# Optimization experiments

Measured on AMD Instinct MI355X. Metric: run time of the kernel, lower is better.

The kernel has to match this reference:

```python
import jax, jax.numpy as jnp
import numpy as np
import math

G = 128          # graphs per batch
N_PER = 512      # nodes per graph (equal-size, contiguous layout)
N = G * N_PER    # 65536 nodes
DEG = 16
E = N * DEG      # 1,048,576 edges
IN_C, HID, OUT_C = 100, 128, 2
RATIO = 0.8
EPS = 1e-5

K1 = int(math.ceil(RATIO * N_PER))  # 410
K2 = int(math.ceil(RATIO * K1))     # 328
K3 = int(math.ceil(RATIO * K2))     # 263


def gcn_conv(x, src, dst, emask, W, b):
    # GCNConv: linear, symmetric deg^-1/2 norm with self-loops, scatter-add
    xl = x @ W
    n = x.shape[0]
    w = emask.astype(x.dtype)
    deg = jnp.ones((n,), x.dtype).at[dst].add(w)      # +1 from self loop
    dinv = jax.lax.rsqrt(deg)
    coef = dinv[src] * dinv[dst] * w                  # [E]
    out = jnp.zeros_like(xl).at[dst].add(coef[:, None] * xl[src])
    out = out + (dinv * dinv)[:, None] * xl           # self-loop messages
    return out + b


def batch_norm(x, gamma, beta):
    # BatchNorm1d over node dim (training-mode batch statistics)
    mu = x.mean(0)
    var = x.var(0)
    return (x - mu) * jax.lax.rsqrt(var + EPS) * gamma + beta


def topk_pool(x, src, dst, emask, att, g, n, k):
    # TopKPooling: score = tanh(x@att/||att||), keep top-k per graph, gate features,
    # drop edges touching removed nodes (via validity mask).
    score = jnp.tanh((x @ att) / jnp.linalg.norm(att))
    _, idx = jax.lax.top_k(score.reshape(g, n), k)           # [g,k] local ids
    kept = (idx + (jnp.arange(g) * n)[:, None]).reshape(-1)   # global ids
    new_x = x[kept] * score[kept][:, None]
    old2new = jnp.full((g * n,), -1, jnp.int32).at[kept].set(
        jnp.arange(g * k, dtype=jnp.int32))
    s2, d2 = old2new[src], old2new[dst]
    valid = emask & (s2 >= 0) & (d2 >= 0)
    return new_x, jnp.maximum(s2, 0), jnp.maximum(d2, 0), valid


def readout(x, g, k):
    # [global_max_pool, global_mean_pool] over each graph's k nodes
    xr = x.reshape(g, k, -1)
    return jnp.concatenate([xr.max(1), xr.mean(1)], axis=1)   # [g, 2C]


def setup_inputs() -> dict:
    key = jax.random.key(0)
    ks = jax.random.split(key, 16)
    x = jax.random.normal(ks[0], (N, IN_C), jnp.float32)
    # within-graph random edges, then offset by graph id
    e_per = E // G
    local = jax.random.randint(ks[1], (2, G, e_per), 0, N_PER)
    edge_index = (local + (jnp.arange(G) * N_PER)[None, :, None]).reshape(2, E).astype(jnp.int32)
    batch = jnp.repeat(jnp.arange(G, dtype=jnp.int32), N_PER)

    def w(k, fi, fo):
        return jax.random.normal(k, (fi, fo), jnp.float32) * (1.0 / np.sqrt(fi))

    z = lambda c: jnp.zeros((c,), jnp.float32)
    o = lambda c: jnp.ones((c,), jnp.float32)
    return {
        'x': x, 'edge_index': edge_index, 'batch': batch,
        'Wp': w(ks[2], IN_C, 128), 'bp': z(128),
        'W1': w(ks[3], 128, HID), 'b1': z(HID), 'g1': o(HID), 'be1': z(HID),
        'att1': jax.random.normal(ks[4], (HID,), jnp.float32),
        'W2': w(ks[5], HID, HID), 'b2': z(HID), 'g2': o(HID), 'be2': z(HID),
        'att2': jax.random.normal(ks[6], (HID,), jnp.float32),
        'W3': w(ks[7], HID, HID), 'b3': z(HID), 'g3': o(HID), 'be3': z(HID),
        'att3': jax.random.normal(ks[8], (HID,), jnp.float32),
        'Wl1': w(ks[9], 2 * HID, HID), 'bl1': z(HID),
        'Wl2': w(ks[10], HID, OUT_C), 'bl2': z(OUT_C),
    }


def reference(x, edge_index, batch, Wp, bp, W1, b1, g1, be1, att1,
              W2, b2, g2, be2, att2, W3, b3, g3, be3, att3,
              Wl1, bl1, Wl2, bl2):
    src, dst = edge_index[0], edge_index[1]
    emask = jnp.ones((E,), bool)
    h = jax.nn.relu(x @ Wp + bp)

    h = jax.nn.relu(batch_norm(gcn_conv(h, src, dst, emask, W1, b1), g1, be1))
    h, src, dst, emask = topk_pool(h, src, dst, emask, att1, G, N_PER, K1)
    x1 = readout(h, G, K1)

    h = jax.nn.relu(batch_norm(gcn_conv(h, src, dst, emask, W2, b2), g2, be2))
    h, src, dst, emask = topk_pool(h, src, dst, emask, att2, G, K1, K2)
    x2 = readout(h, G, K2)

    h = jax.nn.relu(batch_norm(gcn_conv(h, src, dst, emask, W3, b3), g3, be3))
    h, src, dst, emask = topk_pool(h, src, dst, emask, att3, G, K2, K3)
    x3 = readout(h, G, K3)

    s = x1 + x2 + x3                       # [G, 2*HID]
    s = jax.nn.relu(s @ Wl1 + bl1)
    return s @ Wl2 + bl2                   # [G, OUT_C]
```

## Files before the change

### kernel.cpp

```cpp
#include <hip/hip_runtime.h>
#include <math.h>

#define G     128
#define NPER  512
#define NTOT  65536
#define E_TOT 1048576
#define EPG   8192
#define INC   100
#define HID   128
#define KP1   410
#define KP2   328
#define KP3   263

__global__ void init_kernel(short* __restrict__ cmap, float* __restrict__ sread,
                            float* __restrict__ bnpart) {
    int t = blockIdx.x * 256 + threadIdx.x;
    if (t < NTOT) cmap[t] = (short)(t & (NPER - 1));
    if (t < G * 256) { sread[t] = 0.f; bnpart[t] = 0.f; }
}

__global__ __launch_bounds__(512, 2) void csr_build0(
    const int* __restrict__ src, const int* __restrict__ dst,
    unsigned short* __restrict__ csr_g, int* __restrict__ rowptr_g)
{
    __shared__ int cnt_s[NPER];
    __shared__ int rowptr_s[NPER + 1];
    __shared__ int wo_s[NPER];
    __shared__ int chunksum_s[9];

    const int g = blockIdx.x, tid = threadIdx.x, lane = tid & 63, wv = tid >> 6;
    const int ebase = g * EPG, obase = g * NPER;

    cnt_s[tid] = 0;
    __syncthreads();
    for (int e = tid; e < EPG; e += 512)
        atomicAdd(&cnt_s[dst[ebase + e] - obase], 1);
    __syncthreads();

    int v = cnt_s[tid], x = v;
#pragma unroll
    for (int d = 1; d < 64; d <<= 1) {
        int y = __shfl_up(x, d);
        if (lane >= d) x += y;
    }
    if (lane == 63) chunksum_s[wv] = x;
    __syncthreads();
    if (tid == 0) {
        int acc = 0;
#pragma unroll
        for (int k = 0; k < 8; ++k) { int t = chunksum_s[k]; chunksum_s[k] = acc; acc += t; }
    }
    __syncthreads();
    int excl = x - v + chunksum_s[wv];
    rowptr_s[tid] = excl; wo_s[tid] = excl;
    if (tid == 511) rowptr_s[512] = excl + v;
    __syncthreads();

    for (int i = tid; i <= NPER; i += 512) rowptr_g[g * 513 + i] = rowptr_s[i];
    for (int e = tid; e < EPG; e += 512) {
        int sl = src[ebase + e] - obase, dl = dst[ebase + e] - obase;
        int pos = atomicAdd(&wo_s[dl], 1);
        csr_g[g * EPG + pos] = (unsigned short)sl;
    }
}

template<int K, bool RELU>
__global__ __launch_bounds__(256, 2) void gemm_kernel(
    const float* __restrict__ A, const float* __restrict__ W,
    const float* __restrict__ bias, float* __restrict__ out, int M)
{
    constexpr int KC = 32;
    __shared__ float Ws[KC][128];
    __shared__ float As[KC][132];
    const int tid  = threadIdx.x;
    const int row0 = blockIdx.x * 128;
    const int r0 = (tid >> 4) * 8;
    const int c0 = (tid & 15) * 8;

    float acc[8][8];
#pragma unroll
    for (int i = 0; i < 8; ++i)
#pragma unroll
        for (int j = 0; j < 8; ++j) acc[i][j] = 0.f;

    for (int k0 = 0; k0 < K; k0 += KC) {
        const int kc  = (K - k0 < KC) ? (K - k0) : KC;
        const int nf4 = kc >> 2;

        for (int i = tid; i < kc * 32; i += 256) {
            int kk = i >> 5, c4 = i & 31;
            *((float4*)&Ws[kk][0] + c4) =
                *((const float4*)(W + (size_t)(k0 + kk) * 128) + c4);
        }
        for (int i = tid; i < nf4 * 128; i += 256) {
            int row = i / nf4, f4 = i - row * nf4;
            float4 v = *(const float4*)(A + (size_t)(row0 + row) * K + k0 + f4 * 4);
            As[f4 * 4 + 0][row] = v.x;
            As[f4 * 4 + 1][row] = v.y;
            As[f4 * 4 + 2][row] = v.z;
            As[f4 * 4 + 3][row] = v.w;
        }
        __syncthreads();

        for (int kk = 0; kk < kc; ++kk) {
            float4 b0 = *(const float4*)&Ws[kk][c0];
            float4 b1 = *(const float4*)&Ws[kk][c0 + 4];
            float4 a0 = *(const float4*)&As[kk][r0];
            float4 a1 = *(const float4*)&As[kk][r0 + 4];
            float a[8] = {a0.x, a0.y, a0.z, a0.w, a1.x, a1.y, a1.z, a1.w};
            float b[8] = {b0.x, b0.y, b0.z, b0.w, b1.x, b1.y, b1.z, b1.w};
#pragma unroll
            for (int i = 0; i < 8; ++i)
#pragma unroll
                for (int j = 0; j < 8; ++j)
                    acc[i][j] += a[i] * b[j];
        }
        __syncthreads();
    }

#pragma unroll
    for (int i = 0; i < 8; ++i) {
        int row = row0 + r0 + i;
        float o[8];
#pragma unroll
        for (int j = 0; j < 8; ++j) {
            float v = acc[i][j];
            if (RELU) v = fmaxf(v + bias[c0 + j], 0.f);
            o[j] = v;
        }
        float* po = out + (size_t)row * 128 + c0;
        *(float4*)po       = make_float4(o[0], o[1], o[2], o[3]);
        *(float4*)(po + 4) = make_float4(o[4], o[5], o[6], o[7]);
    }
}

template<int NCUR>
__global__ __launch_bounds__(256, 8) void gather_kernel(
    const float* __restrict__ xs, const unsigned short* __restrict__ csr_g,
    const int* __restrict__ rowptr_g, const float* __restrict__ bvec,
    float* __restrict__ out, float* __restrict__ bnpart)
{
    constexpr int CHUNK = (NCUR + 15) / 16;
    constexpr int CSRCAP = 1536;
    __shared__ int   rowptr_s[NCUR + 1];
    __shared__ float dinv_s[NCUR];
    __shared__ unsigned short csr_s[CSRCAP];
    __shared__ float red_s[512];

    const int g = blockIdx.x, s = blockIdx.y;
    const int tid = threadIdx.x, lane = tid & 63, w = tid >> 6;
    const int nbase = g * NCUR;
    const int d0 = s * CHUNK;
    const int d1 = (d0 + CHUNK < NCUR) ? d0 + CHUNK : NCUR;

    const int* rp = rowptr_g + g * 513;
    for (int i = tid; i <= NCUR; i += 256) rowptr_s[i] = rp[i];
    __syncthreads();
    for (int i = tid; i < NCUR; i += 256)
        dinv_s[i] = rsqrtf((float)(rowptr_s[i + 1] - rowptr_s[i] + 1));

    const int base = rowptr_s[d0];
    int nume = rowptr_s[d1] - base;
    if (nume > CSRCAP) nume = CSRCAP;
    const unsigned short* cg = csr_g + g * EPG + base;
    for (int i = tid; i < nume; i += 256) csr_s[i] = cg[i];
    __syncthreads();

    const float2* x2 = (const float2*)xs;
    float2* o2p = (float2*)out;
    const float2 b2 = ((const float2*)bvec)[lane];
    float2 sum = make_float2(0.f, 0.f), sq = make_float2(0.f, 0.f);

    for (int da = d0 + w; da < d1; da += 8) {
        const int db = da + 4;
        const bool hb = db < d1;
        const int ia = rowptr_s[da] - base;
        const int na = rowptr_s[da + 1] - rowptr_s[da];
        const int ib = hb ? rowptr_s[db] - base : 0;
        const int nbl = hb ? rowptr_s[db + 1] - rowptr_s[db] : 0;
        const float dva = dinv_s[da];
        const float dvb = hb ? dinv_s[db] : 0.f;

        float2 xa = x2[(size_t)(nbase + da) * 64 + lane];
        float2 accA = make_float2(dva * xa.x, dva * xa.y);
        float2 accB = make_float2(0.f, 0.f);
        if (hb) {
            float2 xb = x2[(size_t)(nbase + db) * 64 + lane];
            accB = make_float2(dvb * xb.x, dvb * xb.y);
        }

        const int nmin = na < nbl ? na : nbl;
#pragma unroll 2
        for (int t = 0; t < nmin; ++t) {
            int sa = csr_s[ia + t], sb = csr_s[ib + t];
            float wa = dinv_s[sa], wb = dinv_s[sb];
            float2 va = x2[(size_t)(nbase + sa) * 64 + lane];
            float2 vb = x2[(size_t)(nbase + sb) * 64 + lane];
            accA.x += wa * va.x; accA.y += wa * va.y;
            accB.x += wb * vb.x; accB.y += wb * vb.y;
        }
#pragma unroll 4
        for (int t = nmin; t < na; ++t) {
            int sa = csr_s[ia + t];
            float wa = dinv_s[sa];
            float2 va = x2[(size_t)(nbase + sa) * 64 + lane];
            accA.x += wa * va.x; accA.y += wa * va.y;
        }
#pragma unroll 4
        for (int t = nmin; t < nbl; ++t) {
            int sb = csr_s[ib + t];
            float wb = dinv_s[sb];
            float2 vb = x2[(size_t)(nbase + sb) * 64 + lane];
            accB.x += wb * vb.x; accB.y += wb * vb.y;
        }

        float2 oA = make_float2(b2.x + dva * accA.x, b2.y + dva * accA.y);
        o2p[(size_t)(nbase + da) * 64 + lane] = oA;
        sum.x += oA.x; sum.y += oA.y;
        sq.x  += oA.x * oA.x; sq.y += oA.y * oA.y;
        if (hb) {
            float2 oB = make_float2(b2.x + dvb * accB.x, b2.y + dvb * accB.y);
            o2p[(size_t)(nbase + db) * 64 + lane] = oB;
            sum.x += oB.x; sum.y += oB.y;
            sq.x  += oB.x * oB.x; sq.y += oB.y * oB.y;
        }
    }

    float2* red2 = (float2*)red_s;
    red2[tid] = sum; __syncthreads();
    if (tid < 64) {
        float2 a = red2[tid], b_ = red2[tid + 64],
               c = red2[tid + 128], d_ = red2[tid + 192];
        atomicAdd(&bnpart[g * 256 + 2 * tid],     a.x + b_.x + c.x + d_.x);
        atomicAdd(&bnpart[g * 256 + 2 * tid + 1], a.y + b_.y + c.y + d_.y);
    }
    __syncthreads();
    red2[tid] = sq; __syncthreads();
    if (tid < 64) {
        float2 a = red2[tid], b_ = red2[tid + 64],
               c = red2[tid + 128], d_ = red2[tid + 192];
        atomicAdd(&bnpart[g * 256 + 128 + 2 * tid],     a.x + b_.x + c.x + d_.x);
        atomicAdd(&bnpart[g * 256 + 128 + 2 * tid + 1], a.y + b_.y + c.y + d_.y);
    }
}

__global__ __launch_bounds__(1024, 1) void bnfin_kernel(
    const float* __restrict__ bnpart, float n,
    const float* __restrict__ gamma, const float* __restrict__ beta,
    const float* __restrict__ att, float* __restrict__ coefs)
{
    __shared__ float ssum[8][128];
    __shared__ float ssq[8][128];
    __shared__ float r[128];
    const int t = threadIdx.x & 127, slice = threadIdx.x >> 7;
    float s = 0.f, q = 0.f;
    for (int g = slice; g < G; g += 8) {
        s += bnpart[g * 256 + t];
        q += bnpart[g * 256 + 128 + t];
    }
    ssum[slice][t] = s; ssq[slice][t] = q;
    if (threadIdx.x < 128) { float av = att[t]; r[t] = av * av; }
    __syncthreads();
    if (threadIdx.x < 128) {
        float S = 0.f, Q = 0.f;
#pragma unroll
        for (int k = 0; k < 8; ++k) { S += ssum[k][t]; Q += ssq[k][t]; }
        for (int st = 64; st > 0; st >>= 1) {
            if (t < st) r[t] += r[t + st];
            __syncthreads();
        }
        float norm = sqrtf(r[0]);
        float mu   = S / n;
        float var  = Q / n - mu * mu;
        float inv  = rsqrtf(var + 1e-5f);
        float a    = gamma[t] * inv;
        coefs[t]        = a;
        coefs[128 + t]  = beta[t] - mu * a;
        coefs[256 + t]  = att[t] / norm;
    }
}

template<int NCUR, int KK, bool BUILD>
__global__ __launch_bounds__(1024, 1) void pool_kernel(
    const float* __restrict__ gcn, const float* __restrict__ coefs,
    float* __restrict__ newx, short* __restrict__ cmap,
    float* __restrict__ sread, float* __restrict__ bnpart,
    const int* __restrict__ src, const int* __restrict__ dst,
    unsigned short* __restrict__ csr_g, int* __restrict__ rowptr_g)
{
    __shared__ float score_s[NCUR];
    __shared__ unsigned long long key_s[NCUR];
    __shared__ short o2n_s[NCUR];
    __shared__ unsigned short n2o_s[KK];
    __shared__ short cmap_s[NPER];
    __shared__ float2 red2[1024];
    __shared__ int   cnt_s[512];
    __shared__ int   rowptr_s[513];
    __shared__ int   wo_s[512];
    __shared__ int   chunksum_s[9];

    const int g = blockIdx.x, tid = threadIdx.x, lane = tid & 63, w = tid >> 6;
    const int nb = g * NCUR;
    const int ebase = g * EPG, obase = g * NPER;
    const float a0 = coefs[lane],       a1 = coefs[64 + lane];
    const float c0 = coefs[128 + lane], c1 = coefs[192 + lane];
    const float t0 = coefs[256 + lane], t1 = coefs[320 + lane];

    for (int i = tid; i < NPER; i += 1024) cmap_s[i] = cmap[obase + i];

    for (int i = w; i < NCUR; i += 16) {
        const float* row = gcn + (size_t)(nb + i) * 128;
        float h0 = fmaxf(a0 * row[lane] + c0, 0.f);
        float h1 = fmaxf(a1 * row[64 + lane] + c1, 0.f);
        float p  = h0 * t0 + h1 * t1;
#pragma unroll
        for (int off = 32; off > 0; off >>= 1) p += __shfl_down(p, off);
        if (lane == 0) score_s[i] = tanhf(p);
    }
    __syncthreads();

    for (int i = tid; i < NCUR; i += 1024) {
        unsigned u   = __float_as_uint(score_s[i]);
        unsigned key = (u & 0x80000000u) ? ~u : (u | 0x80000000u);
        key_s[i] = ((unsigned long long)key << 32) |
                   (unsigned long long)(0xFFFFFFFFu - (unsigned)i);
    }
    __syncthreads();

    for (int i = tid; i < NCUR; i += 1024) {
        const unsigned long long ki = key_s[i];
        int r = 0;
#pragma unroll 8
        for (int j = 0; j < NCUR; ++j) r += (key_s[j] > ki) ? 1 : 0;
        o2n_s[i] = (r < KK) ? (short)r : (short)-1;
        if (r < KK) n2o_s[r] = (unsigned short)i;
    }
    __syncthreads();

    float mx0 = -1e30f, mx1 = -1e30f, sm0 = 0.f, sm1 = 0.f;
    for (int j2 = w; j2 < KK; j2 += 16) {
        int old = n2o_s[j2];
        float s = score_s[old];
        const float* row = gcn + (size_t)(nb + old) * 128;
        float h0 = fmaxf(a0 * row[lane] + c0, 0.f) * s;
        float h1 = fmaxf(a1 * row[64 + lane] + c1, 0.f) * s;
        float* orow = newx + (size_t)(g * KK + j2) * 128;
        orow[lane]      = h0;
        orow[64 + lane] = h1;
        mx0 = fmaxf(mx0, h0); mx1 = fmaxf(mx1, h1);
        sm0 += h0; sm1 += h1;
    }
    red2[tid] = make_float2(mx0, mx1);
    __syncthreads();
    if (tid < 64) {
        float m = -1e30f;
#pragma unroll
        for (int w2 = 0; w2 < 16; ++w2) m = fmaxf(m, red2[w2 * 64 + tid].x);
        sread[g * 256 + tid] += m;
    } else if (tid < 128) {
        int l = tid - 64;
        float m = -1e30f;
#pragma unroll
        for (int w2 = 0; w2 < 16; ++w2) m = fmaxf(m, red2[w2 * 64 + l].y);
        sread[g * 256 + tid] += m;
    }
    __syncthreads();
    red2[tid] = make_float2(sm0, sm1);
    __syncthreads();
    if (tid < 64) {
        float sm = 0.f;
#pragma unroll
        for (int w2 = 0; w2 < 16; ++w2) sm += red2[w2 * 64 + tid].x;
        sread[g * 256 + 128 + tid] += sm * (1.0f / KK);
    } else if (tid < 128) {
        int l = tid - 64;
        float sm = 0.f;
#pragma unroll
        for (int w2 = 0; w2 < 16; ++w2) sm += red2[w2 * 64 + l].y;
        sread[g * 256 + 128 + tid] += sm * (1.0f / KK);
    }

    for (int o = tid; o < NPER; o += 1024) {
        int m = cmap_s[o];
        short nm = (m >= 0) ? o2n_s[m] : (short)-1;
        cmap_s[o] = nm;
        cmap[obase + o] = nm;
    }
    if (tid < 256) bnpart[g * 256 + tid] = 0.f;

    if (!BUILD) return;
    __syncthreads();

    if (tid < 512) cnt_s[tid] = 0;
    __syncthreads();
    for (int e = tid; e < EPG; e += 1024) {
        int sl = cmap_s[src[ebase + e] - obase];
        int dl = cmap_s[dst[ebase + e] - obase];
        if ((sl | dl) >= 0) atomicAdd(&cnt_s[dl], 1);
    }
    __syncthreads();
    int v = 0, x = 0;
    if (tid < 512) {
        v = cnt_s[tid]; x = v;
#pragma unroll
        for (int d = 1; d < 64; d <<= 1) {
            int y = __shfl_up(x, d);
            if (lane >= d) x += y;
        }
        if (lane == 63) chunksum_s[w] = x;
    }
    __syncthreads();
    if (tid == 0) {
        int acc = 0;
#pragma unroll
        for (int k = 0; k < 8; ++k) { int t = chunksum_s[k]; chunksum_s[k] = acc; acc += t; }
    }
    __syncthreads();
    if (tid < 512) {
        int excl = x - v + chunksum_s[w];
        rowptr_s[tid] = excl; wo_s[tid] = excl;
        if (tid == 511) rowptr_s[512] = excl + v;
    }
    __syncthreads();
    for (int i = tid; i <= 512; i += 1024) rowptr_g[g * 513 + i] = rowptr_s[i];
    for (int e = tid; e < EPG; e += 1024) {
        int sl = cmap_s[src[ebase + e] - obase];
        int dl = cmap_s[dst[ebase + e] - obase];
        if ((sl | dl) >= 0) {
            int pos = atomicAdd(&wo_s[dl], 1);
            csr_g[g * EPG + pos] = (unsigned short)sl;
        }
    }
}

__global__ void final_kernel(const float* __restrict__ sread,
                             const float* __restrict__ Wl1,
                             const float* __restrict__ bl1,
                             const float* __restrict__ Wl2,
                             const float* __restrict__ bl2,
                             float* __restrict__ out)
{
    __shared__ float s_s[256];
    __shared__ float hid_s[128];
    int g = blockIdx.x, t = threadIdx.x;
    s_s[t]       = sread[g * 256 + t];
    s_s[128 + t] = sread[g * 256 + 128 + t];
    __syncthreads();
    float acc = bl1[t];
    for (int i = 0; i < 256; ++i) acc += s_s[i] * Wl1[i * 128 + t];
    hid_s[t] = fmaxf(acc, 0.f);
    __syncthreads();
    if (t < 2) {
        float o = bl2[t];
        for (int j = 0; j < 128; ++j) o += hid_s[j] * Wl2[j * 2 + t];
        out[g * 2 + t] = o;
    }
}

extern "C" void kernel_launch(void* const* d_in, const int* in_sizes, int n_in,
                              void* d_out, int out_size, void* d_ws, size_t ws_size,
                              hipStream_t stream)
{
    const float* x    = (const float*)d_in[0];
    const int*   ei   = (const int*)d_in[1];
    const float* Wp   = (const float*)d_in[3];
    const float* bp   = (const float*)d_in[4];
    const float* W1   = (const float*)d_in[5];
    const float* b1   = (const float*)d_in[6];
    const float* g1   = (const float*)d_in[7];
    const float* be1  = (const float*)d_in[8];
    const float* att1 = (const float*)d_in[9];
    const float* W2   = (const float*)d_in[10];
    const float* b2   = (const float*)d_in[11];
    const float* g2   = (const float*)d_in[12];
    const float* be2  = (const float*)d_in[13];
    const float* att2 = (const float*)d_in[14];
    const float* W3   = (const float*)d_in[15];
    const float* b3   = (const float*)d_in[16];
    const float* g3   = (const float*)d_in[17];
    const float* be3  = (const float*)d_in[18];
    const float* att3 = (const float*)d_in[19];
    const float* Wl1  = (const float*)d_in[20];
    const float* bl1  = (const float*)d_in[21];
    const float* Wl2  = (const float*)d_in[22];
    const float* bl2  = (const float*)d_in[23];
    float* out = (float*)d_out;

    const int* srcp = ei;
    const int* dstp = ei + E_TOT;

    char* ws = (char*)d_ws;
    float*          bufA   = (float*)ws;
    float*          bufB   = (float*)(ws + 33554432);
    unsigned short* csr    = (unsigned short*)(ws + 67108864);
    int*            rowptr = (int*)  (ws + 69206016);
    float*          bnpart = (float*)(ws + 69468672);
    short*          cmap   = (short*)(ws + 69599744);
    float*          sread  = (float*)(ws + 69730816);
    float*          coefs  = (float*)(ws + 69861888);

    init_kernel<<<256, 256, 0, stream>>>(cmap, sread, bnpart);
    csr_build0<<<G, 512, 0, stream>>>(srcp, dstp, csr, rowptr);

    gemm_kernel<INC, true><<<512, 256, 0, stream>>>(x, Wp, bp, bufA, NTOT);

    gemm_kernel<128, false><<<512, 256, 0, stream>>>(bufA, W1, nullptr, bufB, NTOT);
    gather_kernel<512><<<dim3(G, 16), 256, 0, stream>>>(bufB, csr, rowptr, b1, bufA, bnpart);
    bnfin_kernel<<<1, 1024, 0, stream>>>(bnpart, (float)NTOT, g1, be1, att1, coefs);
    pool_kernel<512, KP1, true><<<G, 1024, 0, stream>>>(bufA, coefs, bufB, cmap, sread, bnpart,
                                                        srcp, dstp, csr, rowptr);

    gemm_kernel<128, false><<<410, 256, 0, stream>>>(bufB, W2, nullptr, bufA, G * KP1);
    gather_kernel<KP1><<<dim3(G, 16), 256, 0, stream>>>(bufA, csr, rowptr, b2, bufB, bnpart);
    bnfin_kernel<<<1, 1024, 0, stream>>>(bnpart, (float)(G * KP1), g2, be2, att2, coefs);
    pool_kernel<KP1, KP2, true><<<G, 1024, 0, stream>>>(bufB, coefs, bufA, cmap, sread, bnpart,
                                                        srcp, dstp, csr, rowptr);

    gemm_kernel<128, false><<<328, 256, 0, stream>>>(bufA, W3, nullptr, bufB, G * KP2);
    gather_kernel<KP2><<<dim3(G, 16), 256, 0, stream>>>(bufB, csr, rowptr, b3, bufA, bnpart);
    bnfin_kernel<<<1, 1024, 0, stream>>>(bnpart, (float)(G * KP2), g3, be3, att3, coefs);
    pool_kernel<KP2, KP3, false><<<G, 1024, 0, stream>>>(bufA, coefs, bufB, cmap, sread, bnpart,
                                                         srcp, dstp, csr, rowptr);

    final_kernel<<<G, 128, 0, stream>>>(sread, Wl1, bl1, Wl2, bl2, out);
}
```

Measured before the change: 493.0 us.

## Fold source-side degree norm into GEMM epilogue, fuse BN finalize into pool, double-buffer GEMM

```diff
diff --git a/kernel.cpp b/kernel.cpp
--- a/kernel.cpp
+++ b/kernel.cpp
@@ -16,7 +16,8 @@
                             float* __restrict__ bnpart) {
     int t = blockIdx.x * 256 + threadIdx.x;
     if (t < NTOT) cmap[t] = (short)(t & (NPER - 1));
-    if (t < G * 256) { sread[t] = 0.f; bnpart[t] = 0.f; }
+    if (t < G * 256) sread[t] = 0.f;
+    if (t < 3 * G * 256) bnpart[t] = 0.f;
 }
 
 __global__ __launch_bounds__(512, 2) void csr_build0(
@@ -64,12 +65,11 @@
     }
 }
 
-template<int K, bool RELU>
-__global__ __launch_bounds__(256, 2) void gemm_kernel(
+__global__ __launch_bounds__(256, 2) void gemm_pre(
     const float* __restrict__ A, const float* __restrict__ W,
     const float* __restrict__ bias, float* __restrict__ out, int M)
 {
-    constexpr int KC = 32;
+    constexpr int K = INC, KC = 32;
     __shared__ float Ws[KC][128];
     __shared__ float As[KC][132];
     const int tid  = threadIdx.x;
@@ -102,6 +102,7 @@
         }
         __syncthreads();
 
+#pragma unroll 4
         for (int kk = 0; kk < kc; ++kk) {
             float4 b0 = *(const float4*)&Ws[kk][c0];
             float4 b1 = *(const float4*)&Ws[kk][c0 + 4];
@@ -123,11 +124,127 @@
         int row = row0 + r0 + i;
         float o[8];
 #pragma unroll
-        for (int j = 0; j < 8; ++j) {
-            float v = acc[i][j];
-            if (RELU) v = fmaxf(v + bias[c0 + j], 0.f);
-            o[j] = v;
-        }
+        for (int j = 0; j < 8; ++j)
+            o[j] = fmaxf(acc[i][j] + bias[c0 + j], 0.f);
+        float* po = out + (size_t)row * 128 + c0;
+        *(float4*)po       = make_float4(o[0], o[1], o[2], o[3]);
+        *(float4*)(po + 4) = make_float4(o[4], o[5], o[6], o[7]);
+    }
+}
+
+template<int NCUR>
+__global__ __launch_bounds__(256, 2) void gemm128(
+    const float* __restrict__ A, const float* __restrict__ W,
+    const int* __restrict__ rowptr_g, float* __restrict__ out)
+{
+    constexpr int KC = 32;
+    __shared__ float Ws[2][KC][128];
+    __shared__ float As[2][KC][132];
+    __shared__ float dinv_ls[128];
+    const int tid  = threadIdx.x;
+    const int row0 = blockIdx.x * 128;
+    const int r0 = (tid >> 4) * 8;
+    const int c0 = (tid & 15) * 8;
+
+    if (tid < 128) {
+        int row = row0 + tid;
+        int gg = row / NCUR, ll = row - gg * NCUR;
+        const int* rp = rowptr_g + gg * 513 + ll;
+        dinv_ls[tid] = rsqrtf((float)(rp[1] - rp[0] + 1));
+    }
+
+    const float4* W4 = (const float4*)W;
+
+#pragma unroll
+    for (int j = 0; j < 4; ++j) {
+        int i = tid + j * 256;
+        int kk = i >> 5, c4 = i & 31;
+        *((float4*)&Ws[0][kk][0] + c4) = W4[kk * 32 + c4];
+    }
+#pragma unroll
+    for (int j = 0; j < 4; ++j) {
+        int i = tid + j * 256;
+        int row = i >> 3, f4 = i & 7;
+        float4 v = *(const float4*)(A + (size_t)(row0 + row) * 128 + f4 * 4);
+        As[0][f4 * 4 + 0][row] = v.x;
+        As[0][f4 * 4 + 1][row] = v.y;
+        As[0][f4 * 4 + 2][row] = v.z;
+        As[0][f4 * 4 + 3][row] = v.w;
+    }
+    __syncthreads();
+
+    float acc[8][8];
+#pragma unroll
+    for (int i = 0; i < 8; ++i)
+#pragma unroll
+        for (int j = 0; j < 8; ++j) acc[i][j] = 0.f;
+
+    int p = 0;
+    for (int k0 = 0; k0 < 128; k0 += KC) {
+        const int kn = k0 + KC;
+        const bool has = kn < 128;
+
+        float4 wreg[4], areg[4];
+        if (has) {
+#pragma unroll
+            for (int j = 0; j < 4; ++j) {
+                int i = tid + j * 256;
+                int kk = i >> 5, c4 = i & 31;
+                wreg[j] = W4[(kn + kk) * 32 + c4];
+            }
+#pragma unroll
+            for (int j = 0; j < 4; ++j) {
+                int i = tid + j * 256;
+                int row = i >> 3, f4 = i & 7;
+                areg[j] = *(const float4*)(A + (size_t)(row0 + row) * 128 + kn + f4 * 4);
+            }
+        }
+
+#pragma unroll 4
+        for (int kk = 0; kk < KC; ++kk) {
+            float4 b0 = *(const float4*)&Ws[p][kk][c0];
+            float4 b1 = *(const float4*)&Ws[p][kk][c0 + 4];
+            float4 a0 = *(const float4*)&As[p][kk][r0];
+            float4 a1 = *(const float4*)&As[p][kk][r0 + 4];
+            float a[8] = {a0.x, a0.y, a0.z, a0.w, a1.x, a1.y, a1.z, a1.w};
+            float b[8] = {b0.x, b0.y, b0.z, b0.w, b1.x, b1.y, b1.z, b1.w};
+#pragma unroll
+            for (int i = 0; i < 8; ++i)
+#pragma unroll
+                for (int j = 0; j < 8; ++j)
+                    acc[i][j] += a[i] * b[j];
+        }
+
+        if (has) {
+            int q = p ^ 1;
+#pragma unroll
+            for (int j = 0; j < 4; ++j) {
+                int i = tid + j * 256;
+                int kk = i >> 5, c4 = i & 31;
+                *((float4*)&Ws[q][kk][0] + c4) = wreg[j];
+            }
+#pragma unroll
+            for (int j = 0; j < 4; ++j) {
+                int i = tid + j * 256;
+                int row = i >> 3, f4 = i & 7;
+                float4 v = areg[j];
+                As[q][f4 * 4 + 0][row] = v.x;
+                As[q][f4 * 4 + 1][row] = v.y;
+                As[q][f4 * 4 + 2][row] = v.z;
+                As[q][f4 * 4 + 3][row] = v.w;
+            }
+        }
+        __syncthreads();
+        p ^= 1;
+    }
+
+#pragma unroll
+    for (int i = 0; i < 8; ++i) {
+        int row = row0 + r0 + i;
+        float dv = dinv_ls[r0 + i];
+        float o[8];
+#pragma unroll
+        for (int j = 0; j < 8; ++j) o[j] = acc[i][j] * dv;
         float* po = out + (size_t)row * 128 + c0;
         *(float4*)po       = make_float4(o[0], o[1], o[2], o[3]);
         *(float4*)(po + 4) = make_float4(o[4], o[5], o[6], o[7]);
@@ -142,8 +259,7 @@
 {
     constexpr int CHUNK = (NCUR + 15) / 16;
     constexpr int CSRCAP = 1536;
-    __shared__ int   rowptr_s[NCUR + 1];
-    __shared__ float dinv_s[NCUR];
+    __shared__ int   rowptr_s[CHUNK + 1];
     __shared__ unsigned short csr_s[CSRCAP];
     __shared__ float red_s[512];
 
@@ -152,21 +268,20 @@
     const int nbase = g * NCUR;
     const int d0 = s * CHUNK;
     const int d1 = (d0 + CHUNK < NCUR) ? d0 + CHUNK : NCUR;
-
-    const int* rp = rowptr_g + g * 513;
-    for (int i = tid; i <= NCUR; i += 256) rowptr_s[i] = rp[i];
-    __syncthreads();
-    for (int i = tid; i < NCUR; i += 256)
-        dinv_s[i] = rsqrtf((float)(rowptr_s[i + 1] - rowptr_s[i] + 1));
-
-    const int base = rowptr_s[d0];
-    int nume = rowptr_s[d1] - base;
+    const int len = d1 - d0;
+
+    const int* rp = rowptr_g + g * 513 + d0;
+    for (int i = tid; i <= len; i += 256) rowptr_s[i] = rp[i];
+    __syncthreads();
+
+    const int base = rowptr_s[0];
+    int nume = rowptr_s[len] - base;
     if (nume > CSRCAP) nume = CSRCAP;
     const unsigned short* cg = csr_g + g * EPG + base;
     for (int i = tid; i < nume; i += 256) csr_s[i] = cg[i];
     __syncthreads();
 
-    const float2* x2 = (const float2*)xs;
+    const float2* x2g = (const float2*)xs + (size_t)nbase * 64 + lane;
     float2* o2p = (float2*)out;
     const float2 b2 = ((const float2*)bvec)[lane];
     float2 sum = make_float2(0.f, 0.f), sq = make_float2(0.f, 0.f);
@@ -174,44 +289,36 @@
     for (int da = d0 + w; da < d1; da += 8) {
         const int db = da + 4;
         const bool hb = db < d1;
-        const int ia = rowptr_s[da] - base;
-        const int na = rowptr_s[da + 1] - rowptr_s[da];
-        const int ib = hb ? rowptr_s[db] - base : 0;
-        const int nbl = hb ? rowptr_s[db + 1] - rowptr_s[db] : 0;
-        const float dva = dinv_s[da];
-        const float dvb = hb ? dinv_s[db] : 0.f;
-
-        float2 xa = x2[(size_t)(nbase + da) * 64 + lane];
-        float2 accA = make_float2(dva * xa.x, dva * xa.y);
+        const int ra = da - d0, rb = db - d0;
+        const int ia = rowptr_s[ra] - base;
+        const int na = rowptr_s[ra + 1] - rowptr_s[ra];
+        const int ib = hb ? rowptr_s[rb] - base : 0;
+        const int nbl = hb ? rowptr_s[rb + 1] - rowptr_s[rb] : 0;
+        const float dva = rsqrtf((float)(na + 1));
+        const float dvb = rsqrtf((float)(nbl + 1));
+
+        float2 accA = x2g[(size_t)da * 64];
         float2 accB = make_float2(0.f, 0.f);
-        if (hb) {
-            float2 xb = x2[(size_t)(nbase + db) * 64 + lane];
-            accB = make_float2(dvb * xb.x, dvb * xb.y);
-        }
+        if (hb) accB = x2g[(size_t)db * 64];
 
         const int nmin = na < nbl ? na : nbl;
 #pragma unroll 2
         for (int t = 0; t < nmin; ++t) {
             int sa = csr_s[ia + t], sb = csr_s[ib + t];
-            float wa = dinv_s[sa], wb = dinv_s[sb];
-            float2 va = x2[(size_t)(nbase + sa) * 64 + lane];
-            float2 vb = x2[(size_t)(nbase + sb) * 64 + lane];
-            accA.x += wa * va.x; accA.y += wa * va.y;
-            accB.x += wb * vb.x; accB.y += wb * vb.y;
+            float2 va = x2g[(size_t)sa * 64];
+            float2 vb = x2g[(size_t)sb * 64];
+            accA.x += va.x; accA.y += va.y;
+            accB.x += vb.x; accB.y += vb.y;
         }
 #pragma unroll 4
         for (int t = nmin; t < na; ++t) {
-            int sa = csr_s[ia + t];
-            float wa = dinv_s[sa];
-            float2 va = x2[(size_t)(nbase + sa) * 64 + lane];
-            accA.x += wa * va.x; accA.y += wa * va.y;
+            float2 va = x2g[(size_t)csr_s[ia + t] * 64];
+            accA.x += va.x; accA.y += va.y;
         }
 #pragma unroll 4
         for (int t = nmin; t < nbl; ++t) {
-            int sb = csr_s[ib + t];
-            float wb = dinv_s[sb];
-            float2 vb = x2[(size_t)(nbase + sb) * 64 + lane];
-            accB.x += wb * vb.x; accB.y += wb * vb.y;
+            float2 vb = x2g[(size_t)csr_s[ib + t] * 64];
+            accB.x += vb.x; accB.y += vb.y;
         }
 
         float2 oA = make_float2(b2.x + dva * accA.x, b2.y + dva * accA.y);
@@ -244,50 +351,18 @@
     }
 }
 
-__global__ __launch_bounds__(1024, 1) void bnfin_kernel(
+template<int NCUR, int KK, bool BUILD>
+__global__ __launch_bounds__(1024, 1) void pool_kernel(
+    const float* __restrict__ gcn, float* __restrict__ newx,
+    short* __restrict__ cmap, float* __restrict__ sread,
     const float* __restrict__ bnpart, float n,
     const float* __restrict__ gamma, const float* __restrict__ beta,
-    const float* __restrict__ att, float* __restrict__ coefs)
-{
-    __shared__ float ssum[8][128];
-    __shared__ float ssq[8][128];
-    __shared__ float r[128];
-    const int t = threadIdx.x & 127, slice = threadIdx.x >> 7;
-    float s = 0.f, q = 0.f;
-    for (int g = slice; g < G; g += 8) {
-        s += bnpart[g * 256 + t];
-        q += bnpart[g * 256 + 128 + t];
-    }
-    ssum[slice][t] = s; ssq[slice][t] = q;
-    if (threadIdx.x < 128) { float av = att[t]; r[t] = av * av; }
-    __syncthreads();
-    if (threadIdx.x < 128) {
-        float S = 0.f, Q = 0.f;
-#pragma unroll
-        for (int k = 0; k < 8; ++k) { S += ssum[k][t]; Q += ssq[k][t]; }
-        for (int st = 64; st > 0; st >>= 1) {
-            if (t < st) r[t] += r[t + st];
-            __syncthreads();
-        }
-        float norm = sqrtf(r[0]);
-        float mu   = S / n;
-        float var  = Q / n - mu * mu;
-        float inv  = rsqrtf(var + 1e-5f);
-        float a    = gamma[t] * inv;
-        coefs[t]        = a;
-        coefs[128 + t]  = beta[t] - mu * a;
-        coefs[256 + t]  = att[t] / norm;
-    }
-}
-
-template<int NCUR, int KK, bool BUILD>
-__global__ __launch_bounds__(1024, 1) void pool_kernel(
-    const float* __restrict__ gcn, const float* __restrict__ coefs,
-    float* __restrict__ newx, short* __restrict__ cmap,
-    float* __restrict__ sread, float* __restrict__ bnpart,
+    const float* __restrict__ att,
     const int* __restrict__ src, const int* __restrict__ dst,
     unsigned short* __restrict__ csr_g, int* __restrict__ rowptr_g)
 {
+    __shared__ float coef_s[384];
+    __shared__ float Stmp[128], Qtmp[128], attr[128];
     __shared__ float score_s[NCUR];
     __shared__ unsigned long long key_s[NCUR];
     __shared__ short o2n_s[NCUR];
@@ -302,11 +377,40 @@
     const int g = blockIdx.x, tid = threadIdx.x, lane = tid & 63, w = tid >> 6;
     const int nb = g * NCUR;
     const int ebase = g * EPG, obase = g * NPER;
-    const float a0 = coefs[lane],       a1 = coefs[64 + lane];
-    const float c0 = coefs[128 + lane], c1 = coefs[192 + lane];
-    const float t0 = coefs[256 + lane], t1 = coefs[320 + lane];
-
+
+    if (tid < 128) {
+        float S = 0.f;
+#pragma unroll 4
+        for (int g2 = 0; g2 < G; ++g2) S += bnpart[g2 * 256 + tid];
+        Stmp[tid] = S;
+        float av = att[tid]; attr[tid] = av * av;
+    } else if (tid < 256) {
+        int t = tid - 128;
+        float Q = 0.f;
+#pragma unroll 4
+        for (int g2 = 0; g2 < G; ++g2) Q += bnpart[g2 * 256 + 128 + t];
+        Qtmp[t] = Q;
+    }
     for (int i = tid; i < NPER; i += 1024) cmap_s[i] = cmap[obase + i];
+    __syncthreads();
+    for (int st = 64; st > 0; st >>= 1) {
+        if (tid < st) attr[tid] += attr[tid + st];
+        __syncthreads();
+    }
+    if (tid < 128) {
+        float norm = sqrtf(attr[0]);
+        float mu   = Stmp[tid] / n;
+        float var  = Qtmp[tid] / n - mu * mu;
+        float a    = gamma[tid] * rsqrtf(var + 1e-5f);
+        coef_s[tid]       = a;
+        coef_s[128 + tid] = beta[tid] - mu * a;
+        coef_s[256 + tid] = att[tid] / norm;
+    }
+    __syncthreads();
+
+    const float a0 = coef_s[lane],       a1 = coef_s[64 + lane];
+    const float c0 = coef_s[128 + lane], c1 = coef_s[192 + lane];
+    const float t0 = coef_s[256 + lane], t1 = coef_s[320 + lane];
 
     for (int i = w; i < NCUR; i += 16) {
         const float* row = gcn + (size_t)(nb + i) * 128;
@@ -386,7 +490,6 @@
         cmap_s[o] = nm;
         cmap[obase + o] = nm;
     }
-    if (tid < 256) bnpart[g * 256 + tid] = 0.f;
 
     if (!BUILD) return;
     __syncthreads();
@@ -495,32 +598,35 @@
     unsigned short* csr    = (unsigned short*)(ws + 67108864);
     int*            rowptr = (int*)  (ws + 69206016);
     float*          bnpart = (float*)(ws + 69468672);
-    short*          cmap   = (short*)(ws + 69599744);
-    float*          sread  = (float*)(ws + 69730816);
-    float*          coefs  = (float*)(ws + 69861888);
-
-    init_kernel<<<256, 256, 0, stream>>>(cmap, sread, bnpart);
+    short*          cmap   = (short*)(ws + 69861888);
+    float*          sread  = (float*)(ws + 69992960);
+
+    float* bn0 = bnpart;
+    float* bn1 = bnpart + G * 256;
+    float* bn2 = bnpart + 2 * G * 256;
+
+    init_kernel<<<384, 256, 0, stream>>>(cmap, sread, bnpart);
     csr_build0<<<G, 512, 0, stream>>>(srcp, dstp, csr, rowptr);
 
-    gemm_kernel<INC, true><<<512, 256, 0, stream>>>(x, Wp, bp, bufA, NTOT);
-
-    gemm_kernel<128, false><<<512, 256, 0, stream>>>(bufA, W1, nullptr, bufB, NTOT);
-    gather_kernel<512><<<dim3(G, 16), 256, 0, stream>>>(bufB, csr, rowptr, b1, bufA, bnpart);
-    bnfin_kernel<<<1, 1024, 0, stream>>>(bnpart, (float)NTOT, g1, be1, att1, coefs);
-    pool_kernel<512, KP1, true><<<G, 1024, 0, stream>>>(bufA, coefs, bufB, cmap, sread, bnpart,
-                                                        srcp, dstp, csr, rowptr);
-
-    gemm_kernel<128, false><<<410, 256, 0, stream>>>(bufB, W2, nullptr, bufA, G * KP1);
-    gather_kernel<KP1><<<dim3(G, 16), 256, 0, stream>>>(bufA, csr, rowptr, b2, bufB, bnpart);
-    bnfin_kernel<<<1, 1024, 0, stream>>>(bnpart, (float)(G * KP1), g2, be2, att2, coefs);
-    pool_kernel<KP1, KP2, true><<<G, 1024, 0, stream>>>(bufB, coefs, bufA, cmap, sread, bnpart,
-                                                        srcp, dstp, csr, rowptr);
-
-    gemm_kernel<128, false><<<328, 256, 0, stream>>>(bufA, W3, nullptr, bufB, G * KP2);
-    gather_kernel<KP2><<<dim3(G, 16), 256, 0, stream>>>(bufB, csr, rowptr, b3, bufA, bnpart);
-    bnfin_kernel<<<1, 1024, 0, stream>>>(bnpart, (float)(G * KP2), g3, be3, att3, coefs);
-    pool_kernel<KP2, KP3, false><<<G, 1024, 0, stream>>>(bufA, coefs, bufB, cmap, sread, bnpart,
-                                                         srcp, dstp, csr, rowptr);
+    gemm_pre<<<512, 256, 0, stream>>>(x, Wp, bp, bufA, NTOT);
+
+    gemm128<NPER><<<512, 256, 0, stream>>>(bufA, W1, rowptr, bufB);
+    gather_kernel<NPER><<<dim3(G, 16), 256, 0, stream>>>(bufB, csr, rowptr, b1, bufA, bn0);
+    pool_kernel<NPER, KP1, true><<<G, 1024, 0, stream>>>(
+        bufA, bufB, cmap, sread, bn0, (float)NTOT, g1, be1, att1,
+        srcp, dstp, csr, rowptr);
+
+    gemm128<KP1><<<410, 256, 0, stream>>>(bufB, W2, rowptr, bufA);
+    gather_kernel<KP1><<<dim3(G, 16), 256, 0, stream>>>(bufA, csr, rowptr, b2, bufB, bn1);
+    pool_kernel<KP1, KP2, true><<<G, 1024, 0, stream>>>(
+        bufB, bufA, cmap, sread, bn1, (float)(G * KP1), g2, be2, att2,
+        srcp, dstp, csr, rowptr);
+
+    gemm128<KP2><<<328, 256, 0, stream>>>(bufA, W3, rowptr, bufB);
+    gather_kernel<KP2><<<dim3(G, 16), 256, 0, stream>>>(bufB, csr, rowptr, b3, bufA, bn2);
+    pool_kernel<KP2, KP3, false><<<G, 1024, 0, stream>>>(
+        bufA, bufB, cmap, sread, bn2, (float)(G * KP2), g3, be3, att3,
+        srcp, dstp, csr, rowptr);
 
     final_kernel<<<G, 128, 0, stream>>>(sread, Wl1, bl1, Wl2, bl2, out);
 }
```

New measurement: 494.7 us. About the same (+0.4%).
